# Kernel tuning notes

Hardware: AMD Instinct MI355X
Metric: run time of the kernel (lower is better)

The kernel has to match this reference:

```python
import jax, jax.numpy as jnp
import numpy as np
import math

B, T, D, H = 4, 2048, 1024, 16
HD = D // H  # head dim = 64
ROPE_BASE = 10000.0


def apply_rope(x):
    # x: [b, h, t, hd]. Positions start at 1 (seq_id = arange(1, t+1)) per the source.
    t, hd = x.shape[2], x.shape[3]
    half = hd // 2
    theta = 1.0 / (ROPE_BASE ** (jnp.arange(0, hd, 2, dtype=jnp.float32) / hd))  # [hd/2]
    pos = jnp.arange(1, t + 1, dtype=jnp.float32)  # [t]
    ang = pos[:, None] * theta[None, :]             # [t, hd/2]
    ang = jnp.concatenate([ang, ang], axis=-1)      # [t, hd]
    sin, cos = jnp.sin(ang), jnp.cos(ang)
    # rotate-half: cat([-x2, x1])
    rot = jnp.concatenate([-x[..., half:], x[..., :half]], axis=-1)
    return x * cos[None, None, :, :] + rot * sin[None, None, :, :]


def setup_inputs() -> dict:
    key = jax.random.key(0)
    ks = jax.random.split(key, 9)
    s = 1.0 / math.sqrt(D)
    return {
        "x": jax.random.normal(ks[0], (B, T, D), dtype=jnp.float32),
        "Wq": jax.random.normal(ks[1], (D, D), dtype=jnp.float32) * s,
        "bq": jax.random.normal(ks[2], (D,), dtype=jnp.float32) * 0.01,
        "Wk": jax.random.normal(ks[3], (D, D), dtype=jnp.float32) * s,
        "bk": jax.random.normal(ks[4], (D,), dtype=jnp.float32) * 0.01,
        "Wv": jax.random.normal(ks[5], (D, D), dtype=jnp.float32) * s,
        "bv": jax.random.normal(ks[6], (D,), dtype=jnp.float32) * 0.01,
        "Wo": jax.random.normal(ks[7], (D, D), dtype=jnp.float32) * s,
        "bo": jax.random.normal(ks[8], (D,), dtype=jnp.float32) * 0.01,
    }


def reference(x, Wq, bq, Wk, bk, Wv, bv, Wo, bo):
    b, t, d = x.shape
    h, hd = H, HD
    # projections (torch Linear: x @ W.T + b)
    q = x @ Wq.T + bq
    k = x @ Wk.T + bk
    v = x @ Wv.T + bv
    # [b, t, d] -> [b, h, t, hd]
    split = lambda z: z.reshape(b, t, h, hd).transpose(0, 2, 1, 3)
    q, k, v = split(q), split(k), split(v)
    q = apply_rope(q)
    k = apply_rope(k)
    scale = math.sqrt(hd)
    att = jnp.einsum('bhqd,bhkd->bhqk', q, k) / scale
    mask = jnp.tril(jnp.ones((t, t), dtype=bool))
    att = jnp.where(mask[None, None, :, :], att, -jnp.inf)
    att = jax.nn.softmax(att, axis=-1)
    y = jnp.einsum('bhqk,bhkd->bhqd', att, v)
    y = y.transpose(0, 2, 1, 3).reshape(b, t, d)
    y = y @ Wo.T + bo
    return y
```

## Files before the change

kernel.cpp:

```cpp
#include <hip/hip_runtime.h>

#define BB 4
#define TT 2048
#define DD 1024
#define HH 16
#define HD 64

typedef __attribute__((ext_vector_type(8))) _Float16 f16x8;
typedef __attribute__((ext_vector_type(4))) float f32x4;
typedef __attribute__((ext_vector_type(2))) unsigned int u32x2;
typedef __attribute__((ext_vector_type(4))) unsigned int u32x4;

__device__ __forceinline__ float h2f(unsigned short u) {
    return (float)__builtin_bit_cast(_Float16, u);
}
__device__ __forceinline__ unsigned short f2h(float f) {
    return __builtin_bit_cast(unsigned short, (_Float16)f);
}
__device__ __forceinline__ unsigned int pkrtz(float a, float b) {
    return __builtin_bit_cast(unsigned int, __builtin_amdgcn_cvt_pkrtz(a, b));
}

__global__ __launch_bounds__(256) void conv_all(
    const float4* __restrict__ x,
    const float4* __restrict__ Wq, const float4* __restrict__ Wk,
    const float4* __restrict__ Wv,
    ushort4* __restrict__ xh, ushort4* __restrict__ wh,
    float2* __restrict__ tab)
{
    int vi = blockIdx.x * 256 + threadIdx.x;
    if (vi < 2097152) {
        float4 v = x[vi];
        xh[vi] = (ushort4){ f2h(v.x), f2h(v.y), f2h(v.z), f2h(v.w) };
    } else if (vi < 2883584) {
        int u = vi - 2097152;
        int w = u >> 18;
        const float4* src = (w == 0) ? Wq : (w == 1) ? Wk : Wv;
        float4 v = src[u & 262143];
        wh[u] = (ushort4){ f2h(v.x), f2h(v.y), f2h(v.z), f2h(v.w) };
    } else {
        int u = vi - 2883584;
        int t = u >> 5, i = u & 31;
        float ang = (float)(t + 1) *
                    exp2f(-(float)i * (13.287712379549449f / 32.0f));
        tab[u] = (float2){ cosf(ang), sinf(ang) };
    }
}

__global__ __launch_bounds__(256) void conv_wo(
    const float4* __restrict__ Wo, ushort4* __restrict__ dst)
{
    int i = blockIdx.x * 256 + threadIdx.x;
    float4 v = Wo[i];
    dst[i] = (ushort4){ f2h(v.x), f2h(v.y), f2h(v.z), f2h(v.w) };
}

__global__ __launch_bounds__(256) void gemm_qkv(
    const unsigned short* __restrict__ A,
    const unsigned short* __restrict__ Wall,
    const float* __restrict__ bq, const float* __restrict__ bk,
    const float* __restrict__ bv,
    const float2* __restrict__ tab,
    unsigned short* __restrict__ qkv)
{
    __shared__ __align__(16) unsigned short As[128 * 64];
    __shared__ __align__(16) unsigned short Ws[128 * 64];

    int bid = blockIdx.x;
    int swz = (bid & 7) * 192 + (bid >> 3);
    int bx = swz % 24, by = swz / 24;
    const int sel = bx >> 3;
    const int jb = bx & 7;
    const int n0 = by * 128;
    const int j0 = jb * 128;

    const unsigned short* W = Wall + (size_t)sel * 1048576;
    const float* bias = (sel == 0) ? bq : (sel == 1) ? bk : bv;
    unsigned short* outp = qkv + (size_t)sel * (BB * HH * TT * HD);

    const int tid = threadIdx.x;
    const int w = tid >> 6, lane = tid & 63;
    const int l15 = lane & 15, g = lane >> 4;
    const int wr = w >> 1, wc = w & 1;

    f32x4 acc[4][4];
#pragma unroll
    for (int mi = 0; mi < 4; mi++)
#pragma unroll
        for (int nj = 0; nj < 4; nj++) acc[mi][nj] = (f32x4){0.f, 0.f, 0.f, 0.f};

    u32x4 pa[4], pb[4];
#define LOADREGS(KS)                                                             \
    {                                                                            \
        _Pragma("unroll")                                                        \
        for (int it = 0; it < 4; it++) {                                         \
            int ci = tid + it * 256;                                             \
            int r = ci >> 3, p = ci & 7;                                         \
            pa[it] = *(const u32x4*)(A + (size_t)(n0 + r) * 1024 + (KS) + p * 8);\
            pb[it] = *(const u32x4*)(W + (size_t)(j0 + r) * 1024 + (KS) + p * 8);\
        }                                                                        \
    }

    LOADREGS(0)

    for (int ks = 0; ks < 1024; ks += 64) {
        __syncthreads();
#pragma unroll
        for (int it = 0; it < 4; it++) {
            int ci = tid + it * 256;
            int r = ci >> 3, p = ci & 7;
            int d = r * 64 + ((p ^ (r & 7)) << 3);
            *(u32x4*)(As + d) = pa[it];
            *(u32x4*)(Ws + d) = pb[it];
        }
        __syncthreads();
        if (ks + 64 < 1024) LOADREGS(ks + 64)

#pragma unroll
        for (int c = 0; c < 2; c++) {
            f16x8 af[4], bf[4];
            const int q0c = c * 4 + (g >> 1);
            const int q1c = q0c + 2;
            const int off = (g & 1) << 2;
#pragma unroll
            for (int mi = 0; mi < 4; mi++) {
                int r = wr * 64 + mi * 16 + l15;
                int sw = r & 7;
                const unsigned short* rp = As + r * 64;
                u32x2 x0 = *(const u32x2*)(rp + ((q0c ^ sw) << 3) + off);
                u32x2 x1 = *(const u32x2*)(rp + ((q1c ^ sw) << 3) + off);
                u32x4 uu = {x0.x, x0.y, x1.x, x1.y};
                af[mi] = __builtin_bit_cast(f16x8, uu);
            }
#pragma unroll
            for (int nj = 0; nj < 4; nj++) {
                int r = wc * 64 + nj * 16 + l15;
                int sw = r & 7;
                const unsigned short* rp = Ws + r * 64;
                u32x2 x0 = *(const u32x2*)(rp + ((q0c ^ sw) << 3) + off);
                u32x2 x1 = *(const u32x2*)(rp + ((q1c ^ sw) << 3) + off);
                u32x4 uu = {x0.x, x0.y, x1.x, x1.y};
                bf[nj] = __builtin_bit_cast(f16x8, uu);
            }
#pragma unroll
            for (int mi = 0; mi < 4; mi++)
#pragma unroll
                for (int nj = 0; nj < 4; nj++)
                    acc[mi][nj] = __builtin_amdgcn_mfma_f32_16x16x32_f16(
                        af[mi], bf[nj], acc[mi][nj], 0, 0, 0);
        }
    }
#undef LOADREGS

    float bb4[4];
#pragma unroll
    for (int nj = 0; nj < 4; nj++) bb4[nj] = bias[j0 + wc * 64 + nj * 16 + l15];
    const int hh = (j0 >> 6) + wc;

    if (sel == 2) {
#pragma unroll
        for (int mi = 0; mi < 4; mi++)
#pragma unroll
            for (int r = 0; r < 4; r++) {
                int n = n0 + wr * 64 + mi * 16 + 4 * g + r;
                int b = n >> 11, t = n & (TT - 1);
                size_t rowbase = ((size_t)(b * HH + hh) * TT + t) << 6;
#pragma unroll
                for (int nj = 0; nj < 4; nj++) {
                    int dd = nj * 16 + l15;
                    outp[rowbase + dd] = f2h(acc[mi][nj][r] + bb4[nj]);
                }
            }
    } else {
#pragma unroll
        for (int mi = 0; mi < 4; mi++)
#pragma unroll
            for (int r = 0; r < 4; r++) {
                int n = n0 + wr * 64 + mi * 16 + 4 * g + r;
                int b = n >> 11, t = n & (TT - 1);
                size_t rowbase = ((size_t)(b * HH + hh) * TT + t) << 6;
                const float2* tp = tab + t * 32 + l15;
#pragma unroll
                for (int p = 0; p < 2; p++) {
                    float2 cs = tp[p * 16];
                    float x1 = acc[mi][p][r]     + bb4[p];
                    float x2 = acc[mi][p + 2][r] + bb4[p + 2];
                    int i = p * 16 + l15;
                    outp[rowbase + i]      = f2h(x1 * cs.x - x2 * cs.y);
                    outp[rowbase + i + 32] = f2h(x2 * cs.x + x1 * cs.y);
                }
            }
    }
}

__global__ __launch_bounds__(256) void gemm_h(
    const unsigned short* __restrict__ A, const unsigned short* __restrict__ W,
    const float* __restrict__ bias, float* __restrict__ outp,
    int N, int K, int J)
{
    __shared__ __align__(16) unsigned short As[128 * 64];
    __shared__ __align__(16) unsigned short Ws[128 * 64];

    int total = gridDim.x * gridDim.y;
    int flat = blockIdx.y * gridDim.x + blockIdx.x;
    int swz = (flat & 7) * (total >> 3) + (flat >> 3);
    int bxi = swz % gridDim.x, byi = swz / gridDim.x;

    const int tid = threadIdx.x;
    const int w = tid >> 6, lane = tid & 63;
    const int l15 = lane & 15, g = lane >> 4;
    const int wr = w >> 1, wc = w & 1;
    const int n0 = byi * 128;
    const int j0 = bxi * 128;

    f32x4 acc[4][4];
#pragma unroll
    for (int mi = 0; mi < 4; mi++)
#pragma unroll
        for (int nj = 0; nj < 4; nj++) acc[mi][nj] = (f32x4){0.f, 0.f, 0.f, 0.f};

    u32x4 pa[4], pb[4];
#define LOADREGS(KS)                                                          \
    {                                                                         \
        _Pragma("unroll")                                                     \
        for (int it = 0; it < 4; it++) {                                      \
            int ci = tid + it * 256;                                          \
            int r = ci >> 3, p = ci & 7;                                      \
            pa[it] = *(const u32x4*)(A + (size_t)(n0 + r) * K + (KS) + p * 8);\
            pb[it] = *(const u32x4*)(W + (size_t)(j0 + r) * K + (KS) + p * 8);\
        }                                                                     \
    }

    LOADREGS(0)

    for (int ks = 0; ks < K; ks += 64) {
        __syncthreads();
#pragma unroll
        for (int it = 0; it < 4; it++) {
            int ci = tid + it * 256;
            int r = ci >> 3, p = ci & 7;
            int d = r * 64 + ((p ^ (r & 7)) << 3);
            *(u32x4*)(As + d) = pa[it];
            *(u32x4*)(Ws + d) = pb[it];
        }
        __syncthreads();
        if (ks + 64 < K) LOADREGS(ks + 64)

#pragma unroll
        for (int c = 0; c < 2; c++) {
            f16x8 af[4], bf[4];
            const int q0c = c * 4 + (g >> 1);
            const int q1c = q0c + 2;
            const int off = (g & 1) << 2;
#pragma unroll
            for (int mi = 0; mi < 4; mi++) {
                int r = wr * 64 + mi * 16 + l15;
                int sw = r & 7;
                const unsigned short* rp = As + r * 64;
                u32x2 x0 = *(const u32x2*)(rp + ((q0c ^ sw) << 3) + off);
                u32x2 x1 = *(const u32x2*)(rp + ((q1c ^ sw) << 3) + off);
                u32x4 uu = {x0.x, x0.y, x1.x, x1.y};
                af[mi] = __builtin_bit_cast(f16x8, uu);
            }
#pragma unroll
            for (int nj = 0; nj < 4; nj++) {
                int r = wc * 64 + nj * 16 + l15;
                int sw = r & 7;
                const unsigned short* rp = Ws + r * 64;
                u32x2 x0 = *(const u32x2*)(rp + ((q0c ^ sw) << 3) + off);
                u32x2 x1 = *(const u32x2*)(rp + ((q1c ^ sw) << 3) + off);
                u32x4 uu = {x0.x, x0.y, x1.x, x1.y};
                bf[nj] = __builtin_bit_cast(f16x8, uu);
            }
#pragma unroll
            for (int mi = 0; mi < 4; mi++)
#pragma unroll
                for (int nj = 0; nj < 4; nj++)
                    acc[mi][nj] = __builtin_amdgcn_mfma_f32_16x16x32_f16(
                        af[mi], bf[nj], acc[mi][nj], 0, 0, 0);
        }
    }
#undef LOADREGS

#pragma unroll
    for (int nj = 0; nj < 4; nj++) {
        int j = j0 + wc * 64 + nj * 16 + l15;
        float bb = bias[j];
#pragma unroll
        for (int mi = 0; mi < 4; mi++)
#pragma unroll
            for (int r = 0; r < 4; r++) {
                int n = n0 + wr * 64 + mi * 16 + 4 * g + r;
                outp[(size_t)n * J + j] = acc[mi][nj][r] + bb;
            }
    }
}

__device__ __forceinline__ u32x2 ds_tr16(const unsigned short* p) {
    u32x2 r;
    asm volatile("ds_read_b64_tr_b16 %0, %1"
                 : "=v"(r)
                 : "v"((unsigned int)(unsigned long long)p));
    return r;
}

__global__ __launch_bounds__(256, 4) void attn_mfma(
    const unsigned short* __restrict__ q,
    const unsigned short* __restrict__ k,
    const unsigned short* __restrict__ v,
    unsigned short* __restrict__ aout)
{
    __shared__ __align__(16) unsigned short Ks[64 * 64];
    __shared__ __align__(16) unsigned short Vs[4 * 1056];

    const int h = blockIdx.y, b = blockIdx.z;
    const int tid = threadIdx.x;
    const int w = tid >> 6;
    const int lane = tid & 63;
    const int l15 = lane & 15, g = lane >> 4;
    const int bh = b * HH + h;
    const size_t base = (size_t)bh * TT * 64;
    const unsigned short* Qp = q + base;
    const unsigned short* Kp = k + base;
    const unsigned short* Vp = v + base;

    const float SC = 0.18033688011112042f;

    u32x4 kreg[2];
    u32x2 vreg[4];
#define LOADKV(KB)                                                             \
    {                                                                          \
        _Pragma("unroll")                                                      \
        for (int it = 0; it < 2; it++) {                                       \
            int vi = tid + it * 256;                                           \
            int key = vi >> 3, pr = vi & 7;                                    \
            kreg[it] = *(const u32x4*)(Kp + (size_t)((KB) + key) * 64 + pr * 8);\
        }                                                                      \
        _Pragma("unroll")                                                      \
        for (int it = 0; it < 4; it++) {                                       \
            int vi = tid + it * 256;                                           \
            int key = vi >> 4, c4 = vi & 15;                                   \
            vreg[it] = *(const u32x2*)(Vp + (size_t)((KB) + key) * 64 + c4 * 4);\
        }                                                                      \
    }

    for (int ph = 0; ph < 2; ph++) {
        const int qt = ph ? (31 - (int)blockIdx.x) : (int)blockIdx.x;
        const int q0 = qt * 64;

        f16x8 qf[2];
        {
            const unsigned short* Qr = Qp + (size_t)(q0 + w * 16 + l15) * 64;
#pragma unroll
            for (int c = 0; c < 2; c++) {
                u32x2 a0 = *(const u32x2*)(Qr + 32 * c + 4 * g);
                u32x2 a1 = *(const u32x2*)(Qr + 32 * c + 16 + 4 * g);
                u32x4 uu = {a0.x, a0.y, a1.x, a1.y};
                qf[c] = __builtin_bit_cast(f16x8, uu);
            }
        }

        float mrow = -1e30f, lrow = 0.f;
        f32x4 accO[4];
#pragma unroll
        for (int nb = 0; nb < 4; nb++) accO[nb] = (f32x4){0.f, 0.f, 0.f, 0.f};

        const int ntiles = qt + 1;
        LOADKV(0)

        for (int kt = 0; kt < ntiles; kt++) {
            const bool diag = (kt == qt);
            __syncthreads();
#pragma unroll
            for (int it = 0; it < 2; it++) {
                int vi = tid + it * 256;
                int key = vi >> 3, pr = vi & 7;
                *(u32x4*)(Ks + key * 64 + ((pr ^ (key & 7)) << 3)) = kreg[it];
            }
#pragma unroll
            for (int it = 0; it < 4; it++) {
                int vi = tid + it * 256;
                int key = vi >> 4, c4 = vi & 15;
                *(u32x2*)(Vs + (c4 >> 2) * 1056 + key * 16 + (c4 & 3) * 4) = vreg[it];
            }
            __syncthreads();
            if (kt + 1 < ntiles) LOADKV((kt + 1) * 64)

            const int nkb = diag ? (w + 1) : 4;
            f32x4 accS[4];
#pragma unroll
            for (int kb = 0; kb < 4; kb++) accS[kb] = (f32x4){0.f, 0.f, 0.f, 0.f};
            __builtin_amdgcn_s_setprio(1);
#pragma unroll
            for (int kb = 0; kb < 4; kb++) {
                if (kb < nkb) {
                    int key = kb * 16 + l15;
                    int sw = key & 7;
#pragma unroll
                    for (int c = 0; c < 2; c++) {
                        int c8a = 8 * c + g, c8b = 8 * c + 4 + g;
                        u32x2 x0 = *(const u32x2*)(Ks + key * 64 +
                                       (((c8a >> 1) ^ sw) << 3) + ((c8a & 1) << 2));
                        u32x2 x1 = *(const u32x2*)(Ks + key * 64 +
                                       (((c8b >> 1) ^ sw) << 3) + ((c8b & 1) << 2));
                        u32x4 uu = {x0.x, x0.y, x1.x, x1.y};
                        accS[kb] = __builtin_amdgcn_mfma_f32_16x16x32_f16(
                            __builtin_bit_cast(f16x8, uu), qf[c], accS[kb], 0, 0, 0);
                    }
                }
            }
            __builtin_amdgcn_s_setprio(0);

            float sloc[16];
            float tmax = -1e30f;
            if (diag) {
#pragma unroll
                for (int kb = 0; kb < 4; kb++)
#pragma unroll
                    for (int r = 0; r < 4; r++) {
                        float s = accS[kb][r];
                        bool valid = (kb * 16 + 4 * g + r <= w * 16 + l15);
                        s = valid ? s : -1e30f;
                        sloc[kb * 4 + r] = s;
                        tmax = fmaxf(tmax, s);
                    }
            } else {
#pragma unroll
                for (int kb = 0; kb < 4; kb++)
#pragma unroll
                    for (int r = 0; r < 4; r++) {
                        float s = accS[kb][r];
                        sloc[kb * 4 + r] = s;
                        tmax = fmaxf(tmax, s);
                    }
            }
            tmax = fmaxf(tmax, __shfl_xor(tmax, 16));
            tmax = fmaxf(tmax, __shfl_xor(tmax, 32));

            if (!__all(tmax - mrow <= 61.0f)) {
                float mnew = fmaxf(mrow, tmax);
                float sf = exp2f((mrow - mnew) * SC);
                mrow = mnew;
                lrow *= sf;
                float sfr[4];
#pragma unroll
                for (int r = 0; r < 4; r++) sfr[r] = __shfl(sf, 4 * g + r);
#pragma unroll
                for (int nb = 0; nb < 4; nb++)
#pragma unroll
                    for (int r = 0; r < 4; r++) accO[nb][r] *= sfr[r];
            }

            const float nmsc = -mrow * SC;
            unsigned int pw[8];
            float psum = 0.f;
#pragma unroll
            for (int i = 0; i < 8; i++) {
                float p0 = exp2f(fmaf(sloc[2 * i],     SC, nmsc));
                float p1 = exp2f(fmaf(sloc[2 * i + 1], SC, nmsc));
                pw[i] = pkrtz(p0, p1);
                psum += p0 + p1;
            }
            psum += __shfl_xor(psum, 16);
            psum += __shfl_xor(psum, 32);
            lrow += psum;

            const int nkc = (diag && w < 2) ? 1 : 2;
#pragma unroll
            for (int kc = 0; kc < 2; kc++)
                if (kc < nkc) {
                    u32x2 vfr[4][2];
#pragma unroll
                    for (int nb = 0; nb < 4; nb++)
#pragma unroll
                        for (int t2 = 0; t2 < 2; t2++)
                            vfr[nb][t2] = ds_tr16(
                                Vs + nb * 1056 + (kc * 32 + 16 * t2) * 16 + 4 * lane);
                    asm volatile("s_waitcnt lgkmcnt(0)" ::: "memory");
                    __builtin_amdgcn_sched_barrier(0);
                    u32x4 pu = {pw[4 * kc + 0], pw[4 * kc + 1], pw[4 * kc + 2], pw[4 * kc + 3]};
                    f16x8 pf = __builtin_bit_cast(f16x8, pu);
                    __builtin_amdgcn_s_setprio(1);
#pragma unroll
                    for (int nb = 0; nb < 4; nb++) {
                        u32x4 vu = {vfr[nb][0].x, vfr[nb][0].y,
                                    vfr[nb][1].x, vfr[nb][1].y};
                        accO[nb] = __builtin_amdgcn_mfma_f32_16x16x32_f16(
                            pf, __builtin_bit_cast(f16x8, vu), accO[nb], 0, 0, 0);
                    }
                    __builtin_amdgcn_s_setprio(0);
                }
        }

        float linv = 1.0f / lrow;
        float sfr[4];
#pragma unroll
        for (int r = 0; r < 4; r++) sfr[r] = __shfl(linv, 4 * g + r);
#pragma unroll
        for (int r = 0; r < 4; r++) {
            int qr = q0 + w * 16 + 4 * g + r;
            unsigned short* orow = aout + (size_t)(b * TT + qr) * DD + h * 64;
#pragma unroll
            for (int nb = 0; nb < 4; nb++)
                orow[nb * 16 + l15] = f2h(accO[nb][r] * sfr[r]);
        }
    }
#undef LOADKV
}

extern "C" void kernel_launch(void* const* d_in, const int* in_sizes, int n_in,
                              void* d_out, int out_size, void* d_ws, size_t ws_size,
                              hipStream_t stream)
{
    const float* x  = (const float*)d_in[0];
    const float* Wq = (const float*)d_in[1];
    const float* bq = (const float*)d_in[2];
    const float* Wk = (const float*)d_in[3];
    const float* bk = (const float*)d_in[4];
    const float* Wv = (const float*)d_in[5];
    const float* bv = (const float*)d_in[6];
    const float* Wo = (const float*)d_in[7];
    const float* bo = (const float*)d_in[8];
    float* out = (float*)d_out;

    const size_t NE = (size_t)BB * HH * TT * HD;
    unsigned short* qkv  = (unsigned short*)d_ws;
    unsigned short* qb   = qkv;
    unsigned short* kbuf = qkv + NE;
    unsigned short* vbuf = qkv + 2 * NE;
    float* res = (float*)d_ws;

    unsigned short* ds  = (unsigned short*)d_out;
    unsigned short* xh  = ds;
    unsigned short* wh  = ds + 8388608;
    float2* tab = (float2*)(ds + 11534336);

    const bool direct = ws_size >= (size_t)8 * NE;
    unsigned short* att = direct ? (qkv + 3 * NE) : ds;
    unsigned short* woh = direct ? (unsigned short*)d_ws : (ds + 11796480);
    float* resout = direct ? out : res;

    const int N = BB * TT;
    dim3 blk(256);

    conv_all<<<11520, blk, 0, stream>>>(
        (const float4*)x, (const float4*)Wq, (const float4*)Wk,
        (const float4*)Wv, (ushort4*)xh, (ushort4*)wh, tab);

    gemm_qkv<<<1536, blk, 0, stream>>>(xh, wh, bq, bk, bv, tab, qkv);

    attn_mfma<<<dim3(TT / 128, HH, BB), blk, 0, stream>>>(qb, kbuf, vbuf, att);

    conv_wo<<<1024, blk, 0, stream>>>((const float4*)Wo, (ushort4*)woh);

    gemm_h<<<dim3(DD / 128, N / 128), blk, 0, stream>>>(att, woh, bo, resout, N, DD, DD);

    if (!direct)
        hipMemcpyAsync(out, res, (size_t)N * DD * sizeof(float),
                       hipMemcpyDeviceToDevice, stream);
}
```

Measured before the change: 313.1 us.

## Enlarge attention blocks to 8 waves sharing K/V tiles across 128 query rows

The attention kernel now runs 512-thread blocks covering 128 query rows. Two groups of four waves share each K/V tile staged in LDS, which halves global K/V traffic per query row and spreads the staging loads over more threads. The grid shrinks to 8x16x4 blocks, and each block still handles a mirrored pair of query segments for causal load balance. Waves in the lower query half sit idle on the last key tile. The smaller grid and 512-thread blocks may also lower occupancy.

New measurement: 286.8 us. 8.4% less time.

```diff
diff --git a/kernel.cpp b/kernel.cpp
--- a/kernel.cpp
+++ b/kernel.cpp
@@ -304,7 +304,7 @@
     return r;
 }
 
-__global__ __launch_bounds__(256, 4) void attn_mfma(
+__global__ __launch_bounds__(512, 4) void attn_mfma(
     const unsigned short* __restrict__ q,
     const unsigned short* __restrict__ k,
     const unsigned short* __restrict__ v,
@@ -316,6 +316,8 @@
     const int h = blockIdx.y, b = blockIdx.z;
     const int tid = threadIdx.x;
     const int w = tid >> 6;
+    const int wd = w & 3;
+    const int wt = w >> 2;
     const int lane = tid & 63;
     const int l15 = lane & 15, g = lane >> 4;
     const int bh = b * HH + h;
@@ -326,27 +328,26 @@
 
     const float SC = 0.18033688011112042f;
 
-    u32x4 kreg[2];
-    u32x2 vreg[4];
+    u32x4 kreg;
+    u32x2 vreg[2];
 #define LOADKV(KB)                                                             \
     {                                                                          \
+        {                                                                      \
+            int key = tid >> 3, pr = tid & 7;                                  \
+            kreg = *(const u32x4*)(Kp + (size_t)((KB) + key) * 64 + pr * 8);   \
+        }                                                                      \
         _Pragma("unroll")                                                      \
         for (int it = 0; it < 2; it++) {                                       \
-            int vi = tid + it * 256;                                           \
-            int key = vi >> 3, pr = vi & 7;                                    \
-            kreg[it] = *(const u32x4*)(Kp + (size_t)((KB) + key) * 64 + pr * 8);\
-        }                                                                      \
-        _Pragma("unroll")                                                      \
-        for (int it = 0; it < 4; it++) {                                       \
-            int vi = tid + it * 256;                                           \
+            int vi = tid + it * 512;                                           \
             int key = vi >> 4, c4 = vi & 15;                                   \
             vreg[it] = *(const u32x2*)(Vp + (size_t)((KB) + key) * 64 + c4 * 4);\
         }                                                                      \
     }
 
     for (int ph = 0; ph < 2; ph++) {
-        const int qt = ph ? (31 - (int)blockIdx.x) : (int)blockIdx.x;
-        const int q0 = qt * 64;
+        const int qs = ph ? (15 - (int)blockIdx.x) : (int)blockIdx.x;
+        const int q0 = qs * 128;
+        const int dtile = 2 * qs + wt;
 
         f16x8 qf[2];
         {
@@ -365,131 +366,132 @@
 #pragma unroll
         for (int nb = 0; nb < 4; nb++) accO[nb] = (f32x4){0.f, 0.f, 0.f, 0.f};
 
-        const int ntiles = qt + 1;
+        const int ntiles = 2 * qs + 2;
         LOADKV(0)
 
         for (int kt = 0; kt < ntiles; kt++) {
-            const bool diag = (kt == qt);
+            const bool active = (kt <= dtile);
+            const bool diag = (kt == dtile);
             __syncthreads();
+            {
+                int key = tid >> 3, pr = tid & 7;
+                *(u32x4*)(Ks + key * 64 + ((pr ^ (key & 7)) << 3)) = kreg;
+            }
 #pragma unroll
             for (int it = 0; it < 2; it++) {
-                int vi = tid + it * 256;
-                int key = vi >> 3, pr = vi & 7;
-                *(u32x4*)(Ks + key * 64 + ((pr ^ (key & 7)) << 3)) = kreg[it];
-            }
-#pragma unroll
-            for (int it = 0; it < 4; it++) {
-                int vi = tid + it * 256;
+                int vi = tid + it * 512;
                 int key = vi >> 4, c4 = vi & 15;
                 *(u32x2*)(Vs + (c4 >> 2) * 1056 + key * 16 + (c4 & 3) * 4) = vreg[it];
             }
             __syncthreads();
             if (kt + 1 < ntiles) LOADKV((kt + 1) * 64)
 
-            const int nkb = diag ? (w + 1) : 4;
-            f32x4 accS[4];
-#pragma unroll
-            for (int kb = 0; kb < 4; kb++) accS[kb] = (f32x4){0.f, 0.f, 0.f, 0.f};
-            __builtin_amdgcn_s_setprio(1);
-#pragma unroll
-            for (int kb = 0; kb < 4; kb++) {
-                if (kb < nkb) {
-                    int key = kb * 16 + l15;
-                    int sw = key & 7;
-#pragma unroll
-                    for (int c = 0; c < 2; c++) {
-                        int c8a = 8 * c + g, c8b = 8 * c + 4 + g;
-                        u32x2 x0 = *(const u32x2*)(Ks + key * 64 +
-                                       (((c8a >> 1) ^ sw) << 3) + ((c8a & 1) << 2));
-                        u32x2 x1 = *(const u32x2*)(Ks + key * 64 +
-                                       (((c8b >> 1) ^ sw) << 3) + ((c8b & 1) << 2));
-                        u32x4 uu = {x0.x, x0.y, x1.x, x1.y};
-                        accS[kb] = __builtin_amdgcn_mfma_f32_16x16x32_f16(
-                            __builtin_bit_cast(f16x8, uu), qf[c], accS[kb], 0, 0, 0);
+            if (active) {
+                const int nkb = diag ? (wd + 1) : 4;
+                f32x4 accS[4];
+#pragma unroll
+                for (int kb = 0; kb < 4; kb++) accS[kb] = (f32x4){0.f, 0.f, 0.f, 0.f};
+                __builtin_amdgcn_s_setprio(1);
+#pragma unroll
+                for (int kb = 0; kb < 4; kb++) {
+                    if (kb < nkb) {
+                        int key = kb * 16 + l15;
+                        int sw = key & 7;
+#pragma unroll
+                        for (int c = 0; c < 2; c++) {
+                            int c8a = 8 * c + g, c8b = 8 * c + 4 + g;
+                            u32x2 x0 = *(const u32x2*)(Ks + key * 64 +
+                                           (((c8a >> 1) ^ sw) << 3) + ((c8a & 1) << 2));
+                            u32x2 x1 = *(const u32x2*)(Ks + key * 64 +
+                                           (((c8b >> 1) ^ sw) << 3) + ((c8b & 1) << 2));
+                            u32x4 uu = {x0.x, x0.y, x1.x, x1.y};
+                            accS[kb] = __builtin_amdgcn_mfma_f32_16x16x32_f16(
+                                __builtin_bit_cast(f16x8, uu), qf[c], accS[kb], 0, 0, 0);
+                        }
                     }
                 }
-            }
-            __builtin_amdgcn_s_setprio(0);
-
-            float sloc[16];
-            float tmax = -1e30f;
-            if (diag) {
-#pragma unroll
-                for (int kb = 0; kb < 4; kb++)
-#pragma unroll
-                    for (int r = 0; r < 4; r++) {
-                        float s = accS[kb][r];
-                        bool valid = (kb * 16 + 4 * g + r <= w * 16 + l15);
-                        s = valid ? s : -1e30f;
-                        sloc[kb * 4 + r] = s;
-                        tmax = fmaxf(tmax, s);
+                __builtin_amdgcn_s_setprio(0);
+
+                float sloc[16];
+                float tmax = -1e30f;
+                if (diag) {
+#pragma unroll
+                    for (int kb = 0; kb < 4; kb++)
+#pragma unroll
+                        for (int r = 0; r < 4; r++) {
+                            float s = accS[kb][r];
+                            bool valid = (kb * 16 + 4 * g + r <= wd * 16 + l15);
+                            s = valid ? s : -1e30f;
+                            sloc[kb * 4 + r] = s;
+                            tmax = fmaxf(tmax, s);
+                        }
+                } else {
+#pragma unroll
+                    for (int kb = 0; kb < 4; kb++)
+#pragma unroll
+                        for (int r = 0; r < 4; r++) {
+                            float s = accS[kb][r];
+                            sloc[kb * 4 + r] = s;
+                            tmax = fmaxf(tmax, s);
+                        }
+                }
+                tmax = fmaxf(tmax, __shfl_xor(tmax, 16));
+                tmax = fmaxf(tmax, __shfl_xor(tmax, 32));
+
+                if (!__all(tmax - mrow <= 61.0f)) {
+                    float mnew = fmaxf(mrow, tmax);
+                    float sf = exp2f((mrow - mnew) * SC);
+                    mrow = mnew;
+                    lrow *= sf;
+                    float sfr[4];
+#pragma unroll
+                    for (int r = 0; r < 4; r++) sfr[r] = __shfl(sf, 4 * g + r);
+#pragma unroll
+                    for (int nb = 0; nb < 4; nb++)
+#pragma unroll
+                        for (int r = 0; r < 4; r++) accO[nb][r] *= sfr[r];
+                }
+
+                const float nmsc = -mrow * SC;
+                unsigned int pw[8];
+                float psum = 0.f;
+#pragma unroll
+                for (int i = 0; i < 8; i++) {
+                    float p0 = exp2f(fmaf(sloc[2 * i],     SC, nmsc));
+                    float p1 = exp2f(fmaf(sloc[2 * i + 1], SC, nmsc));
+                    pw[i] = pkrtz(p0, p1);
+                    psum += p0 + p1;
+                }
+                psum += __shfl_xor(psum, 16);
+                psum += __shfl_xor(psum, 32);
+                lrow += psum;
+
+                const int nkc = (diag && wd < 2) ? 1 : 2;
+#pragma unroll
+                for (int kc = 0; kc < 2; kc++)
+                    if (kc < nkc) {
+                        u32x2 vfr[4][2];
+#pragma unroll
+                        for (int nb = 0; nb < 4; nb++)
+#pragma unroll
+                            for (int t2 = 0; t2 < 2; t2++)
+                                vfr[nb][t2] = ds_tr16(
+                                    Vs + nb * 1056 + (kc * 32 + 16 * t2) * 16 + 4 * lane);
+                        asm volatile("s_waitcnt lgkmcnt(0)" ::: "memory");
+                        __builtin_amdgcn_sched_barrier(0);
+                        u32x4 pu = {pw[4 * kc + 0], pw[4 * kc + 1], pw[4 * kc + 2], pw[4 * kc + 3]};
+                        f16x8 pf = __builtin_bit_cast(f16x8, pu);
+                        __builtin_amdgcn_s_setprio(1);
+#pragma unroll
+                        for (int nb = 0; nb < 4; nb++) {
+                            u32x4 vu = {vfr[nb][0].x, vfr[nb][0].y,
+                                        vfr[nb][1].x, vfr[nb][1].y};
+                            accO[nb] = __builtin_amdgcn_mfma_f32_16x16x32_f16(
+                                pf, __builtin_bit_cast(f16x8, vu), accO[nb], 0, 0, 0);
+                        }
+                        __builtin_amdgcn_s_setprio(0);
                     }
-            } else {
-#pragma unroll
-                for (int kb = 0; kb < 4; kb++)
-#pragma unroll
-                    for (int r = 0; r < 4; r++) {
-                        float s = accS[kb][r];
-                        sloc[kb * 4 + r] = s;
-                        tmax = fmaxf(tmax, s);
-                    }
-            }
-            tmax = fmaxf(tmax, __shfl_xor(tmax, 16));
-            tmax = fmaxf(tmax, __shfl_xor(tmax, 32));
-
-            if (!__all(tmax - mrow <= 61.0f)) {
-                float mnew = fmaxf(mrow, tmax);
-                float sf = exp2f((mrow - mnew) * SC);
-                mrow = mnew;
-                lrow *= sf;
-                float sfr[4];
-#pragma unroll
-                for (int r = 0; r < 4; r++) sfr[r] = __shfl(sf, 4 * g + r);
-#pragma unroll
-                for (int nb = 0; nb < 4; nb++)
-#pragma unroll
-                    for (int r = 0; r < 4; r++) accO[nb][r] *= sfr[r];
-            }
-
-            const float nmsc = -mrow * SC;
-            unsigned int pw[8];
-            float psum = 0.f;
-#pragma unroll
-            for (int i = 0; i < 8; i++) {
-                float p0 = exp2f(fmaf(sloc[2 * i],     SC, nmsc));
-                float p1 = exp2f(fmaf(sloc[2 * i + 1], SC, nmsc));
-                pw[i] = pkrtz(p0, p1);
-                psum += p0 + p1;
-            }
-            psum += __shfl_xor(psum, 16);
-            psum += __shfl_xor(psum, 32);
-            lrow += psum;
-
-            const int nkc = (diag && w < 2) ? 1 : 2;
-#pragma unroll
-            for (int kc = 0; kc < 2; kc++)
-                if (kc < nkc) {
-                    u32x2 vfr[4][2];
-#pragma unroll
-                    for (int nb = 0; nb < 4; nb++)
-#pragma unroll
-                        for (int t2 = 0; t2 < 2; t2++)
-                            vfr[nb][t2] = ds_tr16(
-                                Vs + nb * 1056 + (kc * 32 + 16 * t2) * 16 + 4 * lane);
-                    asm volatile("s_waitcnt lgkmcnt(0)" ::: "memory");
-                    __builtin_amdgcn_sched_barrier(0);
-                    u32x4 pu = {pw[4 * kc + 0], pw[4 * kc + 1], pw[4 * kc + 2], pw[4 * kc + 3]};
-                    f16x8 pf = __builtin_bit_cast(f16x8, pu);
-                    __builtin_amdgcn_s_setprio(1);
-#pragma unroll
-                    for (int nb = 0; nb < 4; nb++) {
-                        u32x4 vu = {vfr[nb][0].x, vfr[nb][0].y,
-                                    vfr[nb][1].x, vfr[nb][1].y};
-                        accO[nb] = __builtin_amdgcn_mfma_f32_16x16x32_f16(
-                            pf, __builtin_bit_cast(f16x8, vu), accO[nb], 0, 0, 0);
-                    }
-                    __builtin_amdgcn_s_setprio(0);
-                }
+            }
         }
 
         float linv = 1.0f / lrow;
@@ -549,7 +551,7 @@
 
     gemm_qkv<<<1536, blk, 0, stream>>>(xh, wh, bq, bk, bv, tab, qkv);
 
-    attn_mfma<<<dim3(TT / 128, HH, BB), blk, 0, stream>>>(qb, kbuf, vbuf, att);
+    attn_mfma<<<dim3(8, HH, BB), dim3(512), 0, stream>>>(qb, kbuf, vbuf, att);
 
     conv_wo<<<1024, blk, 0, stream>>>((const float4*)Wo, (ushort4*)woh);
 
```
